# Kernel tuning notes

Hardware: AMD Instinct MI355X
Metric: run time of the kernel (lower is better)

The kernel has to match this reference:

```python
import jax, jax.numpy as jnp
import numpy as np

N = 50000          # nodes
E = 1_600_000      # edges (avg degree 32)
IN = 128           # in_channels
H1, C1 = 4, 8      # conv1: heads=4, out=8 -> concat 32
OUT = 64           # out_channels (conv2, heads=1)
NEG_SLOPE = 0.2    # PyG GATConv default LeakyReLU slope


def _gat_layer(x, edge_index, W, att_src, att_dst, bias, heads, out_ch):
    """PyG-style GATConv (concat=True, add_self_loops=True).
    x: [N, F_in], edge_index: [2, E], W: [F_in, heads*out_ch],
    att_src/att_dst: [heads, out_ch], bias: [heads*out_ch].
    """
    n = x.shape[0]
    loops = jnp.arange(n)
    src = jnp.concatenate([edge_index[0], loops])  # message source j
    dst = jnp.concatenate([edge_index[1], loops])  # aggregation target i

    h = (x @ W).reshape(n, heads, out_ch)                 # [N, H, C]
    a_src = jnp.sum(h * att_src, axis=-1)                 # [N, H]
    a_dst = jnp.sum(h * att_dst, axis=-1)                 # [N, H]

    logits = jax.nn.leaky_relu(a_src[src] + a_dst[dst], NEG_SLOPE)  # [E', H]
    # segment softmax over incoming edges of each destination node
    m = jax.ops.segment_max(logits, dst, num_segments=n)            # [N, H]
    e = jnp.exp(logits - m[dst])
    s = jax.ops.segment_sum(e, dst, num_segments=n)                 # [N, H]
    alpha = e / (s[dst] + 1e-16)                                    # [E', H]

    msg = h[src] * alpha[..., None]                                 # [E', H, C]
    out = jax.ops.segment_sum(msg, dst, num_segments=n)             # [N, H, C]
    return out.reshape(n, heads * out_ch) + bias


def setup_inputs() -> dict:
    key = jax.random.key(0)
    ks = jax.random.split(key, 10)
    g = 0.1
    x = jax.random.normal(ks[0], (N, IN), jnp.float32)
    edge_index = jax.random.randint(ks[1], (2, E), 0, N, dtype=jnp.int64)
    W1 = jax.random.normal(ks[2], (IN, H1 * C1), jnp.float32) * g
    att_src1 = jax.random.normal(ks[3], (H1, C1), jnp.float32) * g
    att_dst1 = jax.random.normal(ks[4], (H1, C1), jnp.float32) * g
    b1 = jnp.zeros((H1 * C1,), jnp.float32)
    W2 = jax.random.normal(ks[5], (H1 * C1, OUT), jnp.float32) * g
    att_src2 = jax.random.normal(ks[6], (1, OUT), jnp.float32) * g
    att_dst2 = jax.random.normal(ks[7], (1, OUT), jnp.float32) * g
    b2 = jnp.zeros((OUT,), jnp.float32)
    return {"x": x, "edge_index": edge_index,
            "W1": W1, "att_src1": att_src1, "att_dst1": att_dst1, "b1": b1,
            "W2": W2, "att_src2": att_src2, "att_dst2": att_dst2, "b2": b2}


def reference(x, edge_index, W1, att_src1, att_dst1, b1, W2, att_src2, att_dst2, b2):
    h = _gat_layer(x, edge_index, W1, att_src1, att_dst1, b1, H1, C1)   # [N, 32]
    h = jax.nn.relu(h)
    out = _gat_layer(h, edge_index, W2, att_src2, att_dst2, b2, 1, OUT)  # [N, 64]
    return out
```

## Files before the change

### kernel.cpp

```cpp
#include <hip/hip_runtime.h>
#include <hip/hip_bf16.h>

#define IN_CH 128
#define H1C1  32
#define NH1   4
#define OUTC  64
#define NEG   0.2f
#define RPAD  8
#define BSH   6
#define BSZ   64
#define NBMAX 1024
#define CHUNK 4096
#define CAP   3072
#define PCAP  3584

typedef __hip_bfloat16 bf16;
typedef unsigned int u32;
typedef unsigned short u16;

__device__ __forceinline__ u16 f2bf_bits(float f) {
  bf16 v = __float2bfloat16(f);
  return *(u16*)&v;
}
__device__ __forceinline__ float bflo(u32 g) { return __uint_as_float(g << 16); }
__device__ __forceinline__ float bfhi(u32 g) { return __uint_as_float(g & 0xFFFF0000u); }


__global__ __launch_bounds__(256) void k_bin(
    const int* __restrict__ ei, int* __restrict__ bucket_fill,
    u32* __restrict__ data, int E, int n, int nb) {
  __shared__ int cnt[NBMAX];
  __shared__ int lbase[NBMAX];
  __shared__ int gbase[NBMAX];
  __shared__ u32 staged[CHUNK];
  int t = threadIdx.x;
  int lane = t & 63, wid = t >> 6;
  for (int b = t; b < nb; b += 256) cnt[b] = 0;
  __syncthreads();
  long base = (long)blockIdx.x * CHUNK;
  long totE = (long)E + n;
  u32 pk[CHUNK / 256];
  int bk[CHUNK / 256];
#pragma unroll
  for (int i = 0; i < CHUNK / 256; i++) {
    long e = base + i * 256 + t;
    if (e < totE) {
      int j, d;
      if (e < E) {
        j = ei[e]; d = ei[E + e];
        j = j < 0 ? 0 : (j >= n ? n - 1 : j);
        d = d < 0 ? 0 : (d >= n ? n - 1 : d);
      } else { j = d = (int)(e - E); }
      bk[i] = d >> BSH;
      pk[i] = ((u32)d << 16) | (u32)j;
      atomicAdd(&cnt[bk[i]], 1);
    } else bk[i] = -1;
  }
  __syncthreads();
  if (wid == 0) {
    int carry = 0;
    for (int b0 = 0; b0 < nb; b0 += 64) {
      int i = b0 + lane;
      int v = (i < nb) ? cnt[i] : 0;
      int orig = v;
      for (int off = 1; off < 64; off <<= 1) {
        int u = __shfl_up(v, off, 64);
        if (lane >= off) v += u;
      }
      if (i < nb) lbase[i] = carry + v - orig;
      carry += __shfl(v, 63, 64);
    }
  }
  __syncthreads();
  for (int b = t; b < nb; b += 256) {
    int c = cnt[b];
    gbase[b] = c ? atomicAdd(&bucket_fill[b], c) : 0;
    cnt[b] = 0;
  }
  __syncthreads();
#pragma unroll
  for (int i = 0; i < CHUNK / 256; i++) {
    if (bk[i] >= 0) {
      int loc = atomicAdd(&cnt[bk[i]], 1);
      staged[lbase[bk[i]] + loc] = pk[i];
    }
  }
  __syncthreads();
  long remL = totE - base;
  int rem = remL > CHUNK ? CHUNK : (int)remL;
  for (int idx = t; idx < rem; idx += 256) {
    u32 p = staged[idx];
    int b = (int)(p >> 16) >> BSH;
    int off2 = gbase[b] + (idx - lbase[b]);
    if (off2 < CAP) data[(size_t)b * CAP + off2] = p;
  }
}

__global__ __launch_bounds__(256) void k_bucket_scatter(
    const u32* __restrict__ data, const int* __restrict__ bucket_fill,
    int2* __restrict__ rowse, int* __restrict__ col, int n) {
  __shared__ int cur[BSZ];
  __shared__ int rp[BSZ];
  __shared__ int pd[BSZ];
  int t = threadIdx.x;
  int b = blockIdx.x;
  if (t < BSZ) cur[t] = 0;
  __syncthreads();
  int s = b * CAP;
  int cnt = bucket_fill[b];
  if (cnt > CAP) cnt = CAP;
  for (int i = t; i < cnt; i += 256)
    atomicAdd(&cur[(data[s + i] >> 16) & (BSZ - 1)], 1);
  __syncthreads();
  if (t < 64) {
    int raw = cur[t];
    int v = (raw + RPAD - 1) & ~(RPAD - 1);
    int orig = v;
    for (int off = 1; off < 64; off <<= 1) {
      int u = __shfl_up(v, off, 64);
      if (t >= off) v += u;
    }
    int r = b * PCAP + v - orig;
    rp[t] = r;
    pd[t] = orig;
    cur[t] = r;
    int node = (b << BSH) + t;
    if (node < n) rowse[node] = make_int2(r, r + orig);
  }
  __syncthreads();
  for (int i = t; i < cnt; i += 256) {
    u32 p = data[s + i];
    int dl = (int)(p >> 16) & (BSZ - 1);
    int pos = atomicAdd(&cur[dl], 1);
    col[pos] = (int)(p & 0xFFFFu);
  }
  __syncthreads();
  if (t < 64) {
    int c = cur[t];
    int end = rp[t] + pd[t];
    for (int k = c; k < end; k++) col[k] = n;
  }
}

__global__ __launch_bounds__(256) void k_l1_transform(
    const float* __restrict__ x, const float* __restrict__ W1,
    const float* __restrict__ as1, const float* __restrict__ ad1,
    u16* __restrict__ h1b, float* __restrict__ a_src, float* __restrict__ a_dst,
    int n) {
  __shared__ float W1s[32 * 128];
  __shared__ float xs[8 * IN_CH];
  int t = threadIdx.x;
  for (int idx = t; idx < IN_CH * H1C1; idx += 256) {
    int k = idx >> 5, m = idx & 31;
    W1s[(k >> 2) * 128 + m * 4 + (k & 3)] = W1[idx];
  }
  int base = blockIdx.x * 8;
  for (int idx = t; idx < 8 * IN_CH; idx += 256) {
    int row = idx >> 7, k = idx & 127;
    int nb = base + row;
    xs[idx] = (nb < n) ? x[(size_t)nb * IN_CH + k] : 0.f;
  }
  __syncthreads();
  int nl = t >> 5, m = t & 31;
  int node = base + nl;
  float acc = 0.f;
#pragma unroll
  for (int kg = 0; kg < 32; kg++) {
    float4 xv = *(const float4*)(xs + nl * IN_CH + kg * 4);
    float4 wv = *(const float4*)(W1s + kg * 128 + m * 4);
    acc += xv.x * wv.x + xv.y * wv.y + xv.z * wv.z + xv.w * wv.w;
  }
  float vs = acc * as1[m];
  float vd = acc * ad1[m];
  for (int off = 1; off < 8; off <<= 1) {
    vs += __shfl_xor(vs, off, 64);
    vd += __shfl_xor(vd, off, 64);
  }
  if (node < n) {
    h1b[node * H1C1 + m] = f2bf_bits(acc);
    if ((m & 7) == 0) {
      a_src[node * NH1 + (m >> 3)] = vs;
      a_dst[node * NH1 + (m >> 3)] = vd;
    }
  }
  if (blockIdx.x == 0) {
    if (t < H1C1) h1b[n * H1C1 + t] = 0;
    if (t < NH1)  a_src[n * NH1 + t] = -1e30f;
  }
}

__global__ __launch_bounds__(256) void k_l1_agg(
    const int2* __restrict__ rowse, const int* __restrict__ col,
    const u16* __restrict__ h1b, const float* __restrict__ a_src,
    const float* __restrict__ a_dst, const float* __restrict__ b1,
    const float* __restrict__ W2, const float* __restrict__ as2,
    const float* __restrict__ ad2,
    u16* __restrict__ h2, float* __restrict__ a_src2, float* __restrict__ a_dst2,
    int n) {
  __shared__ float W2s[8 * 256];
  __shared__ float hsh[4][H1C1];
  __shared__ int   js[4][64];
  __shared__ float wsh[4][NH1][64];
  int t = threadIdx.x;
  int wid = t >> 6, lane = t & 63;
  for (int idx = t; idx < H1C1 * OUTC; idx += 256) {
    int k = idx >> 6, c = idx & 63;
    W2s[(k >> 2) * 256 + c * 4 + (k & 3)] = W2[idx];
  }
  int node = blockIdx.x * 4 + wid;
  int q = lane >> 4, u = lane & 15;
  int hd = u >> 2;
  if (node < n) {
    int2 se = rowse[node];
    int rs = se.x, re = se.y;
    float4 ad = *(const float4*)(a_dst + node * NH1);
    float a0 = 0.f, a1 = 0.f, sw = 0.f;
    for (int tb = rs; tb < re; tb += 64) {
      int kmax = re - tb; if (kmax > 64) kmax = 64;
      if (lane < kmax) {
        int j = col[tb + lane];
        float4 as = *(const float4*)(a_src + j * NH1);
        float l0 = as.x + ad.x; l0 = l0 > 0.f ? l0 : NEG * l0;
        float l1 = as.y + ad.y; l1 = l1 > 0.f ? l1 : NEG * l1;
        float l2 = as.z + ad.z; l2 = l2 > 0.f ? l2 : NEG * l2;
        float l3 = as.w + ad.w; l3 = l3 > 0.f ? l3 : NEG * l3;
        js[wid][lane] = j;
        wsh[wid][0][lane] = __expf(l0);
        wsh[wid][1][lane] = __expf(l1);
        wsh[wid][2][lane] = __expf(l2);
        wsh[wid][3][lane] = __expf(l3);
      }
      for (int k = 2 * q; k < kmax; k += 8) {
        int2 j2 = *(const int2*)(&js[wid][k]);
        float2 wv = *(const float2*)(&wsh[wid][hd][k]);
        u32 g0 = *(const u32*)(h1b + j2.x * H1C1 + 2 * u);
        u32 g1 = *(const u32*)(h1b + j2.y * H1C1 + 2 * u);
        a0 += wv.x * bflo(g0) + wv.y * bflo(g1);
        a1 += wv.x * bfhi(g0) + wv.y * bfhi(g1);
        sw += wv.x + wv.y;
      }
    }
    a0 += __shfl_xor(a0, 16, 64); a0 += __shfl_xor(a0, 32, 64);
    a1 += __shfl_xor(a1, 16, 64); a1 += __shfl_xor(a1, 32, 64);
    sw += __shfl_xor(sw, 16, 64); sw += __shfl_xor(sw, 32, 64);
    if (q == 0) {
      float inv = 1.f / (sw + 1e-16f);
      int c = 2 * u;
      hsh[wid][c]     = fmaxf(a0 * inv + b1[c], 0.f);
      hsh[wid][c + 1] = fmaxf(a1 * inv + b1[c + 1], 0.f);
    }
  }
  __syncthreads();
  float acc = 0.f;
#pragma unroll
  for (int kg = 0; kg < 8; kg++) {
    float4 hv = *(const float4*)(&hsh[wid][kg * 4]);
    float4 wv = *(const float4*)(W2s + kg * 256 + lane * 4);
    acc += hv.x * wv.x + hv.y * wv.y + hv.z * wv.z + hv.w * wv.w;
  }
  float vs = acc * as2[lane];
  float vd = acc * ad2[lane];
  for (int off = 1; off < 64; off <<= 1) {
    vs += __shfl_xor(vs, off, 64);
    vd += __shfl_xor(vd, off, 64);
  }
  if (node < n) {
    h2[node * OUTC + lane] = f2bf_bits(acc);
    if (lane == 0) { a_src2[node] = vs; a_dst2[node] = vd; }
  }
  if (blockIdx.x == 0) {
    if (t < OUTC) h2[n * OUTC + t] = 0;
    if (t == 0)   a_src2[n] = -1e30f;
  }
}

__global__ __launch_bounds__(256) void k_l2_agg(
    const int2* __restrict__ rowse, const int* __restrict__ col,
    const u16* __restrict__ h2, const float* __restrict__ a_src2,
    const float* __restrict__ a_dst2, const float* __restrict__ b2v,
    float* __restrict__ out, int n) {
  __shared__ int   js[4][64];
  __shared__ float wsh[4][64];
  int t = threadIdx.x;
  int wid = t >> 6, lane = t & 63;
  int node = blockIdx.x * 4 + wid;
  if (node >= n) return;
  int h = lane >> 5, u = lane & 31;
  int2 se = rowse[node];
  int rs = se.x, re = se.y;
  float ad = a_dst2[node];
  float a0 = 0.f, a1 = 0.f, sw = 0.f;
  for (int tb = rs; tb < re; tb += 64) {
    int kmax = re - tb; if (kmax > 64) kmax = 64;
    if (lane < kmax) {
      int j = col[tb + lane];
      float lg = a_src2[j] + ad;
      lg = lg > 0.f ? lg : NEG * lg;
      js[wid][lane] = j;
      wsh[wid][lane] = __expf(lg);
    }
    for (int k = 4 * h; k < kmax; k += 8) {
      int4 j4 = *(const int4*)(&js[wid][k]);
      float4 wv = *(const float4*)(&wsh[wid][k]);
      u32 g0 = *(const u32*)(h2 + j4.x * OUTC + 2 * u);
      u32 g1 = *(const u32*)(h2 + j4.y * OUTC + 2 * u);
      u32 g2 = *(const u32*)(h2 + j4.z * OUTC + 2 * u);
      u32 g3 = *(const u32*)(h2 + j4.w * OUTC + 2 * u);
      a0 += wv.x * bflo(g0) + wv.y * bflo(g1);
      a0 += wv.z * bflo(g2) + wv.w * bflo(g3);
      a1 += wv.x * bfhi(g0) + wv.y * bfhi(g1);
      a1 += wv.z * bfhi(g2) + wv.w * bfhi(g3);
      sw += (wv.x + wv.y) + (wv.z + wv.w);
    }
  }
  a0 += __shfl_xor(a0, 32, 64);
  a1 += __shfl_xor(a1, 32, 64);
  sw += __shfl_xor(sw, 32, 64);
  if (h == 0) {
    float inv = 1.f / (sw + 1e-16f);
    int c = 2 * u;
    float2 o;
    o.x = a0 * inv + b2v[c];
    o.y = a1 * inv + b2v[c + 1];
    *(float2*)(out + node * OUTC + c) = o;
  }
}


extern "C" void kernel_launch(void* const* d_in, const int* in_sizes, int n_in,
                              void* d_out, int out_size, void* d_ws, size_t ws_size,
                              hipStream_t stream) {
  const float* x   = (const float*)d_in[0];
  const int*   ei  = (const int*)d_in[1];
  const float* W1  = (const float*)d_in[2];
  const float* as1 = (const float*)d_in[3];
  const float* ad1 = (const float*)d_in[4];
  const float* b1  = (const float*)d_in[5];
  const float* W2  = (const float*)d_in[6];
  const float* as2 = (const float*)d_in[7];
  const float* ad2 = (const float*)d_in[8];
  const float* b2  = (const float*)d_in[9];
  float* out = (float*)d_out;

  int n = in_sizes[0] / IN_CH;
  int E = in_sizes[1] / 2;
  int nb = (n + BSZ - 1) >> BSH;
  long tot = (long)E + n;
  int nA = (int)((tot + CHUNK - 1) / CHUNK);

  char* w = (char*)d_ws;
  auto al = [](size_t v) { return (v + 255) & ~(size_t)255; };
  size_t off = 0;
  int*  bucket_fill = (int*)(w + off);  off += al((size_t)nb * 4);
  int2* rowse       = (int2*)(w + off); off += al((size_t)(n + 1) * 8);
  u32*  data        = (u32*)(w + off);  off += al((size_t)nb * CAP * 4);
  int*  col         = (int*)(w + off);  off += al((size_t)nb * PCAP * 4);
  u16*  h1b         = (u16*)(w + off);  off += al((size_t)(n + 1) * H1C1 * 2);
  float* a_src1     = (float*)(w + off); off += al((size_t)(n + 1) * NH1 * 4);
  float* a_dst1     = (float*)(w + off); off += al((size_t)(n + 1) * NH1 * 4);
  u16*  h2          = (u16*)(w + off);  off += al((size_t)(n + 1) * OUTC * 2);
  float* a_src2     = (float*)(w + off); off += al((size_t)(n + 1) * 4);
  float* a_dst2     = (float*)(w + off); off += al((size_t)(n + 1) * 4);

  hipMemsetAsync(bucket_fill, 0, (size_t)nb * 4, stream);
  hipLaunchKernelGGL(k_bin, dim3(nA), dim3(256), 0, stream,
                     ei, bucket_fill, data, E, n, nb);
  hipLaunchKernelGGL(k_bucket_scatter, dim3(nb), dim3(256), 0, stream,
                     data, bucket_fill, rowse, col, n);

  hipLaunchKernelGGL(k_l1_transform, dim3((n + 7) / 8), dim3(256), 0, stream,
                     x, W1, as1, ad1, h1b, a_src1, a_dst1, n);
  hipLaunchKernelGGL(k_l1_agg, dim3((n + 3) / 4), dim3(256), 0, stream,
                     rowse, col, h1b, a_src1, a_dst1, b1,
                     W2, as2, ad2, h2, a_src2, a_dst2, n);

  hipLaunchKernelGGL(k_l2_agg, dim3((n + 3) / 4), dim3(256), 0, stream,
                     rowse, col, h2, a_src2, a_dst2, b2, out, n);
}
```

Baseline: 222.9 us.

## Process four nodes per wave in GAT aggregation kernels to amortize W2 staging

Each wave in both aggregation kernels now handles four destination nodes in sequence instead of one, so each block covers 16 nodes and the grid shrinks fourfold. In k_l1_agg this spreads the 8 KB per-block W2 shared-memory staging over four times as many nodes. That staging is also rewritten as float4 stores, and the softmax weight buffer is padded to reduce LDS bank conflicts. The cost is fewer blocks in flight and sequential per-wave node processing, which may reduce latency hiding and load balance across nodes of differing degree.

Measured after the change: 224.8 us. About the same (+0.8%).

```diff
diff --git a/kernel.cpp b/kernel.cpp
--- a/kernel.cpp
+++ b/kernel.cpp
@@ -198,19 +198,29 @@
     u16* __restrict__ h2, float* __restrict__ a_src2, float* __restrict__ a_dst2,
     int n) {
   __shared__ float W2s[8 * 256];
-  __shared__ float hsh[4][H1C1];
+  __shared__ float hsh[16][H1C1];
   __shared__ int   js[4][64];
-  __shared__ float wsh[4][NH1][64];
+  __shared__ float wsh[4][NH1][68];
   int t = threadIdx.x;
   int wid = t >> 6, lane = t & 63;
-  for (int idx = t; idx < H1C1 * OUTC; idx += 256) {
-    int k = idx >> 6, c = idx & 63;
-    W2s[(k >> 2) * 256 + c * 4 + (k & 3)] = W2[idx];
-  }
-  int node = blockIdx.x * 4 + wid;
+  {
+    int c = t & 63;
+#pragma unroll
+    for (int g = 0; g < 2; g++) {
+      int kg = (t >> 6) + 4 * g;
+      float4 v;
+      v.x = W2[(kg * 4 + 0) * OUTC + c];
+      v.y = W2[(kg * 4 + 1) * OUTC + c];
+      v.z = W2[(kg * 4 + 2) * OUTC + c];
+      v.w = W2[(kg * 4 + 3) * OUTC + c];
+      *(float4*)(W2s + kg * 256 + c * 4) = v;
+    }
+  }
   int q = lane >> 4, u = lane & 15;
   int hd = u >> 2;
-  if (node < n) {
+  for (int s = 0; s < 4; s++) {
+    int node = blockIdx.x * 16 + wid * 4 + s;
+    if (node >= n) continue;
     int2 se = rowse[node];
     int rs = se.x, re = se.y;
     float4 ad = *(const float4*)(a_dst + node * NH1);
@@ -246,27 +256,32 @@
     if (q == 0) {
       float inv = 1.f / (sw + 1e-16f);
       int c = 2 * u;
-      hsh[wid][c]     = fmaxf(a0 * inv + b1[c], 0.f);
-      hsh[wid][c + 1] = fmaxf(a1 * inv + b1[c + 1], 0.f);
-    }
-  }
-  __syncthreads();
-  float acc = 0.f;
-#pragma unroll
-  for (int kg = 0; kg < 8; kg++) {
-    float4 hv = *(const float4*)(&hsh[wid][kg * 4]);
-    float4 wv = *(const float4*)(W2s + kg * 256 + lane * 4);
-    acc += hv.x * wv.x + hv.y * wv.y + hv.z * wv.z + hv.w * wv.w;
-  }
-  float vs = acc * as2[lane];
-  float vd = acc * ad2[lane];
-  for (int off = 1; off < 64; off <<= 1) {
-    vs += __shfl_xor(vs, off, 64);
-    vd += __shfl_xor(vd, off, 64);
-  }
-  if (node < n) {
-    h2[node * OUTC + lane] = f2bf_bits(acc);
-    if (lane == 0) { a_src2[node] = vs; a_dst2[node] = vd; }
+      hsh[wid * 4 + s][c]     = fmaxf(a0 * inv + b1[c], 0.f);
+      hsh[wid * 4 + s][c + 1] = fmaxf(a1 * inv + b1[c + 1], 0.f);
+    }
+  }
+  __syncthreads();
+  float as2l = as2[lane], ad2l = ad2[lane];
+  for (int r = 0; r < 4; r++) {
+    int nl = wid * 4 + r;
+    int node = blockIdx.x * 16 + nl;
+    float acc = 0.f;
+#pragma unroll
+    for (int kg = 0; kg < 8; kg++) {
+      float4 hv = *(const float4*)(&hsh[nl][kg * 4]);
+      float4 wv = *(const float4*)(W2s + kg * 256 + lane * 4);
+      acc += hv.x * wv.x + hv.y * wv.y + hv.z * wv.z + hv.w * wv.w;
+    }
+    float vs = acc * as2l;
+    float vd = acc * ad2l;
+    for (int off = 1; off < 64; off <<= 1) {
+      vs += __shfl_xor(vs, off, 64);
+      vd += __shfl_xor(vd, off, 64);
+    }
+    if (node < n) {
+      h2[node * OUTC + lane] = f2bf_bits(acc);
+      if (lane == 0) { a_src2[node] = vs; a_dst2[node] = vd; }
+    }
   }
   if (blockIdx.x == 0) {
     if (t < OUTC) h2[n * OUTC + t] = 0;
@@ -283,46 +298,48 @@
   __shared__ float wsh[4][64];
   int t = threadIdx.x;
   int wid = t >> 6, lane = t & 63;
-  int node = blockIdx.x * 4 + wid;
-  if (node >= n) return;
   int h = lane >> 5, u = lane & 31;
-  int2 se = rowse[node];
-  int rs = se.x, re = se.y;
-  float ad = a_dst2[node];
-  float a0 = 0.f, a1 = 0.f, sw = 0.f;
-  for (int tb = rs; tb < re; tb += 64) {
-    int kmax = re - tb; if (kmax > 64) kmax = 64;
-    if (lane < kmax) {
-      int j = col[tb + lane];
-      float lg = a_src2[j] + ad;
-      lg = lg > 0.f ? lg : NEG * lg;
-      js[wid][lane] = j;
-      wsh[wid][lane] = __expf(lg);
-    }
-    for (int k = 4 * h; k < kmax; k += 8) {
-      int4 j4 = *(const int4*)(&js[wid][k]);
-      float4 wv = *(const float4*)(&wsh[wid][k]);
-      u32 g0 = *(const u32*)(h2 + j4.x * OUTC + 2 * u);
-      u32 g1 = *(const u32*)(h2 + j4.y * OUTC + 2 * u);
-      u32 g2 = *(const u32*)(h2 + j4.z * OUTC + 2 * u);
-      u32 g3 = *(const u32*)(h2 + j4.w * OUTC + 2 * u);
-      a0 += wv.x * bflo(g0) + wv.y * bflo(g1);
-      a0 += wv.z * bflo(g2) + wv.w * bflo(g3);
-      a1 += wv.x * bfhi(g0) + wv.y * bfhi(g1);
-      a1 += wv.z * bfhi(g2) + wv.w * bfhi(g3);
-      sw += (wv.x + wv.y) + (wv.z + wv.w);
-    }
-  }
-  a0 += __shfl_xor(a0, 32, 64);
-  a1 += __shfl_xor(a1, 32, 64);
-  sw += __shfl_xor(sw, 32, 64);
-  if (h == 0) {
-    float inv = 1.f / (sw + 1e-16f);
-    int c = 2 * u;
-    float2 o;
-    o.x = a0 * inv + b2v[c];
-    o.y = a1 * inv + b2v[c + 1];
-    *(float2*)(out + node * OUTC + c) = o;
+  for (int s = 0; s < 4; s++) {
+    int node = blockIdx.x * 16 + wid * 4 + s;
+    if (node >= n) continue;
+    int2 se = rowse[node];
+    int rs = se.x, re = se.y;
+    float ad = a_dst2[node];
+    float a0 = 0.f, a1 = 0.f, sw = 0.f;
+    for (int tb = rs; tb < re; tb += 64) {
+      int kmax = re - tb; if (kmax > 64) kmax = 64;
+      if (lane < kmax) {
+        int j = col[tb + lane];
+        float lg = a_src2[j] + ad;
+        lg = lg > 0.f ? lg : NEG * lg;
+        js[wid][lane] = j;
+        wsh[wid][lane] = __expf(lg);
+      }
+      for (int k = 4 * h; k < kmax; k += 8) {
+        int4 j4 = *(const int4*)(&js[wid][k]);
+        float4 wv = *(const float4*)(&wsh[wid][k]);
+        u32 g0 = *(const u32*)(h2 + j4.x * OUTC + 2 * u);
+        u32 g1 = *(const u32*)(h2 + j4.y * OUTC + 2 * u);
+        u32 g2 = *(const u32*)(h2 + j4.z * OUTC + 2 * u);
+        u32 g3 = *(const u32*)(h2 + j4.w * OUTC + 2 * u);
+        a0 += wv.x * bflo(g0) + wv.y * bflo(g1);
+        a0 += wv.z * bflo(g2) + wv.w * bflo(g3);
+        a1 += wv.x * bfhi(g0) + wv.y * bfhi(g1);
+        a1 += wv.z * bfhi(g2) + wv.w * bfhi(g3);
+        sw += (wv.x + wv.y) + (wv.z + wv.w);
+      }
+    }
+    a0 += __shfl_xor(a0, 32, 64);
+    a1 += __shfl_xor(a1, 32, 64);
+    sw += __shfl_xor(sw, 32, 64);
+    if (h == 0) {
+      float inv = 1.f / (sw + 1e-16f);
+      int c = 2 * u;
+      float2 o;
+      o.x = a0 * inv + b2v[c];
+      o.y = a1 * inv + b2v[c + 1];
+      *(float2*)(out + node * OUTC + c) = o;
+    }
   }
 }
 
@@ -370,10 +387,10 @@
 
   hipLaunchKernelGGL(k_l1_transform, dim3((n + 7) / 8), dim3(256), 0, stream,
                      x, W1, as1, ad1, h1b, a_src1, a_dst1, n);
-  hipLaunchKernelGGL(k_l1_agg, dim3((n + 3) / 4), dim3(256), 0, stream,
+  hipLaunchKernelGGL(k_l1_agg, dim3((n + 15) / 16), dim3(256), 0, stream,
                      rowse, col, h1b, a_src1, a_dst1, b1,
                      W2, as2, ad2, h2, a_src2, a_dst2, n);
 
-  hipLaunchKernelGGL(k_l2_agg, dim3((n + 3) / 4), dim3(256), 0, stream,
+  hipLaunchKernelGGL(k_l2_agg, dim3((n + 15) / 16), dim3(256), 0, stream,
                      rowse, col, h2, a_src2, a_dst2, b2, out, n);
 }
```
